# Performance work log

Measured on AMD Instinct MI355X. Metric: run time of the kernel, lower is better.

## Reference

```python
import jax, jax.numpy as jnp
import numpy as np

SIZE_DICT = 1024
DIM_DICT = 256
BETA = 0.001


def setup_inputs() -> dict:
    key = jax.random.key(0)
    k1, k2 = jax.random.split(key)
    z = jax.random.normal(k1, (64, 1024, DIM_DICT), dtype=jnp.float32)
    codebook = jax.random.normal(k2, (SIZE_DICT, DIM_DICT), dtype=jnp.float32)
    return {"z": z, "codebook": codebook, "flg_train": 1}


def reference(z, codebook, flg_train):
    zf = z.reshape(-1, DIM_DICT)  # [N, D]
    # squared euclidean distances: ||z||^2 + ||c||^2 - 2 z c^T  -> [N, K]
    d = (jnp.sum(zf ** 2, axis=1, keepdims=True)
         + jnp.sum(codebook ** 2, axis=1)
         - 2.0 * jnp.matmul(zf, codebook.T))
    idx = jnp.argmin(d, axis=1)  # [N]
    # one-hot @ codebook == gather
    z_q = codebook[idx].reshape(z.shape)
    if flg_train:
        loss = (jnp.mean((jax.lax.stop_gradient(z_q) - z) ** 2)
                + BETA * jnp.mean((z_q - jax.lax.stop_gradient(z)) ** 2))
    else:
        loss = jnp.float32(0.0)
    # straight-through estimator
    z_q = z + jax.lax.stop_gradient(z_q - z)
    # perplexity from codebook usage histogram (== mean of one-hot rows)
    n = zf.shape[0]
    counts = jax.ops.segment_sum(jnp.ones((n,), jnp.float32), idx,
                                 num_segments=SIZE_DICT)
    e_mean = counts / n
    perplexity = jnp.exp(-jnp.sum(e_mean * jnp.log(e_mean + 1e-10)))
    return (z_q, loss, perplexity)
```

## Files before the change

kernel.cpp:

```cpp
#include <hip/hip_runtime.h>


#define N_ROWS 65536
#define DIM    256
#define K_CODES 1024
#define BETA   0.001f

#define BM      128
#define NBLOCKS (N_ROWS / BM)
#define NTHREADS 512
#define STAGE_BYTES 32768
#define NSTAGE  32

#define LO_SCALE 2048.0f
#define LO_INV   (1.0f / 2048.0f)

#define WS_CBIMG_OFF 16384
#define WS_NEED (WS_CBIMG_OFF + NSTAGE * STAGE_BYTES)

typedef _Float16 f16x8 __attribute__((ext_vector_type(8)));
typedef float f32x16 __attribute__((ext_vector_type(16)));


__global__ void cnorm_kernel(const float* __restrict__ cb, float* __restrict__ cnorm) {
    int k = blockIdx.x * blockDim.x + threadIdx.x;
    if (k >= K_CODES) return;
    const float4* row = (const float4*)(cb + (size_t)k * DIM);
    float s = 0.f;
#pragma unroll
    for (int j = 0; j < DIM / 4; ++j) {
        float4 v = row[j];
        s = fmaf(v.x, v.x, s);
        s = fmaf(v.y, v.y, s);
        s = fmaf(v.z, v.z, s);
        s = fmaf(v.w, v.w, s);
    }
    cnorm[k] = s;
}

__global__ void cb_prep(const float* __restrict__ cb, char* __restrict__ img) {
    int idx = blockIdx.x * blockDim.x + threadIdx.x;
    int c   = idx >> 5;
    int g32 = idx & 31;
    const float4* src = (const float4*)(cb + (size_t)c * DIM + g32 * 8);
    float4 v0 = src[0], v1 = src[1];
    float vv[8] = {v0.x, v0.y, v0.z, v0.w, v1.x, v1.y, v1.z, v1.w};
    f16x8 hi, lo;
#pragma unroll
    for (int j = 0; j < 8; ++j) {
        _Float16 h = (_Float16)vv[j];
        hi[j] = h;
        lo[j] = (_Float16)((vv[j] - (float)h) * LO_SCALE);
    }
    int kh = g32 >> 4;
    int gl = g32 & 15;
    int cl = c & 63;
    int gp = gl ^ (cl & 7);
    int unit = (c >> 6) * 2 + kh;
    size_t off = (size_t)unit * STAGE_BYTES + (size_t)cl * 256 + (size_t)gp * 16;
    *(f16x8*)(img + off) = hi;
    *(f16x8*)(img + off + 16384) = lo;
}


__device__ inline void stage_unit(const char* img, int u, char* ldsbase, int tid) {
#pragma unroll
    for (int i = 0; i < 4; ++i) {
        __builtin_amdgcn_global_load_lds(
            (const __attribute__((address_space(1))) unsigned int*)
                (img + (size_t)u * STAGE_BYTES + i * 8192 + tid * 16),
            (__attribute__((address_space(3))) unsigned int*)
                (ldsbase + i * 8192 + tid * 16),
            16, 0, 0);
    }
}

#define COMPUTE_HALF(KH, BUF)                                                        \
    {                                                                                \
        const _Float16* ch_row = csb + (BUF) * 16384 + crow * 128;                   \
        const _Float16* cl_row = ch_row + 8192;                                      \
        _Pragma("unroll")                                                            \
        for (int ks = 0; ks < 8; ++ks) {                                             \
            int gb = (ks * 2 + lh) ^ csw;                                            \
            f16x8 bh = *(const f16x8*)(ch_row + gb * 8);                             \
            f16x8 bl = *(const f16x8*)(cl_row + gb * 8);                             \
            f16x8 ah = zh[(KH) * 8 + ks];                                            \
            f16x8 al = zl[(KH) * 8 + ks];                                            \
            acc_hh = __builtin_amdgcn_mfma_f32_32x32x16_f16(ah, bh, acc_hh, 0, 0, 0);\
            f32x16& ax = (ks & 1) ? acc_xo : acc_xe;                                 \
            ax = __builtin_amdgcn_mfma_f32_32x32x16_f16(ah, bl, ax, 0, 0, 0);        \
            ax = __builtin_amdgcn_mfma_f32_32x32x16_f16(al, bh, ax, 0, 0, 0);        \
        }                                                                            \
    }

__global__ __launch_bounds__(NTHREADS, 2)
void vq_main_mfma(const float* __restrict__ z, const float* __restrict__ cb,
                  const char* __restrict__ img, const float* __restrict__ cnorm,
                  float* __restrict__ out, int* __restrict__ counts,
                  float* __restrict__ ploss) {
    __shared__ _Float16 csb[2 * 16384];
    __shared__ unsigned long long bkey2[BM][2];
    __shared__ int bests[BM];
    __shared__ float red[NTHREADS];

    const int tid  = threadIdx.x;
    const int lane = tid & 63;
    const int w    = tid >> 6;
    const int wr   = w >> 1;
    const int wc   = w & 1;
    const int l31  = lane & 31;
    const int lh   = lane >> 5;
    const int r0   = blockIdx.x * BM;

    stage_unit(img, 0, (char*)csb, tid);

    const int zrow = wr * 32 + l31;
    f16x8 zh[16], zl[16];
    {
        const float* zr = z + (size_t)(r0 + zrow) * DIM;
#pragma unroll
        for (int gi = 0; gi < 16; ++gi) {
            int g = gi * 2 + lh;
            float4 v0 = *(const float4*)(zr + g * 8);
            float4 v1 = *(const float4*)(zr + g * 8 + 4);
            float vv[8] = {v0.x, v0.y, v0.z, v0.w, v1.x, v1.y, v1.z, v1.w};
            f16x8 hi, lo;
#pragma unroll
            for (int j = 0; j < 8; ++j) {
                _Float16 h = (_Float16)vv[j];
                hi[j] = h;
                lo[j] = (_Float16)((vv[j] - (float)h) * LO_SCALE);
            }
            zh[gi] = hi;
            zl[gi] = lo;
        }
    }

    f32x16 acc_hh, acc_xe, acc_xo;
#pragma unroll
    for (int e = 0; e < 16; ++e) { acc_hh[e] = 0.f; acc_xe[e] = 0.f; acc_xo[e] = 0.f; }
    unsigned long long bestk[16];
#pragma unroll
    for (int e = 0; e < 16; ++e) bestk[e] = ~0ull;

    const int crow = wc * 32 + l31;
    const int csw  = crow & 7;

#pragma unroll 1
    for (int chunk = 0; chunk < 16; ++chunk) {
        asm volatile("" ::: "memory");
        __builtin_amdgcn_s_barrier();
        asm volatile("" ::: "memory");
        stage_unit(img, 2 * chunk + 1, (char*)csb + 32768, tid);
        asm volatile("s_waitcnt vmcnt(4)" ::: "memory");
        __builtin_amdgcn_s_barrier();
        asm volatile("" ::: "memory");
        __builtin_amdgcn_s_setprio(1);
        COMPUTE_HALF(0, 0)
        __builtin_amdgcn_s_setprio(0);

        asm volatile("" ::: "memory");
        __builtin_amdgcn_s_barrier();
        asm volatile("" ::: "memory");
        if (chunk + 1 < 16) {
            stage_unit(img, 2 * chunk + 2, (char*)csb, tid);
            asm volatile("s_waitcnt vmcnt(4)" ::: "memory");
        } else {
            asm volatile("s_waitcnt vmcnt(0)" ::: "memory");
        }
        __builtin_amdgcn_s_barrier();
        asm volatile("" ::: "memory");
        __builtin_amdgcn_s_setprio(1);
        COMPUTE_HALF(1, 1)
        __builtin_amdgcn_s_setprio(0);

        {
            int col = chunk * 64 + wc * 32 + l31;
            float cn = cnorm[col];
#pragma unroll
            for (int rg = 0; rg < 16; ++rg) {
                float dot = fmaf(acc_xe[rg] + acc_xo[rg], LO_INV, acc_hh[rg]);
                float s = fmaf(-2.0f, dot, cn);
                unsigned uu = __float_as_uint(s);
                uu = (uu & 0x80000000u) ? ~uu : (uu | 0x80000000u);
                unsigned long long key = ((unsigned long long)uu << 32) | (unsigned)col;
                bestk[rg] = key < bestk[rg] ? key : bestk[rg];
            }
#pragma unroll
            for (int e = 0; e < 16; ++e) { acc_hh[e] = 0.f; acc_xe[e] = 0.f; acc_xo[e] = 0.f; }
        }
    }

#pragma unroll
    for (int rg = 0; rg < 16; ++rg) {
        unsigned long long bk = bestk[rg];
#pragma unroll
        for (int s = 1; s < 32; s <<= 1) {
            unsigned long long o = __shfl_xor(bk, s, 64);
            bk = o < bk ? o : bk;
        }
        bestk[rg] = bk;
    }
    if (l31 == 0) {
#pragma unroll
        for (int rg = 0; rg < 16; ++rg) {
            int rl = (rg & 3) + 8 * (rg >> 2) + 4 * lh;
            bkey2[wr * 32 + rl][wc] = bestk[rg];
        }
    }
    __syncthreads();
    if (tid < BM) {
        unsigned long long a = bkey2[tid][0];
        unsigned long long b2 = bkey2[tid][1];
        bests[tid] = (int)((a < b2 ? a : b2) & 0xffffffffu);
    }
    __syncthreads();

    const int r = tid >> 2;
    const int q = tid & 3;
    const int bidx = bests[r];
    const float* crow_g = cb + (size_t)bidx * DIM;
    const float* zrow_g = z + (size_t)(r0 + r) * DIM;
    float* orow = out + (size_t)(r0 + r) * DIM;
    float lsum = 0.f;
#pragma unroll
    for (int j = 0; j < 16; ++j) {
        int g4 = j * 4 + q;
        float4 c4 = *(const float4*)(crow_g + g4 * 4);
        float4 z4 = *(const float4*)(zrow_g + g4 * 4);
        float4 o;
        float dx = c4.x - z4.x; o.x = z4.x + dx; lsum = fmaf(dx, dx, lsum);
        float dy = c4.y - z4.y; o.y = z4.y + dy; lsum = fmaf(dy, dy, lsum);
        float dz = c4.z - z4.z; o.z = z4.z + dz; lsum = fmaf(dz, dz, lsum);
        float dw = c4.w - z4.w; o.w = z4.w + dw; lsum = fmaf(dw, dw, lsum);
        *(float4*)(orow + g4 * 4) = o;
    }
    if (tid < BM) atomicAdd(&counts[bests[tid]], 1);

    red[tid] = lsum;
    __syncthreads();
    for (int s = NTHREADS / 2; s > 0; s >>= 1) {
        if (tid < s) red[tid] += red[tid + s];
        __syncthreads();
    }
    if (tid == 0) ploss[blockIdx.x] = red[0];
}


#define FBM     32
#define FCHUNK  512
#define FDSTAGE 16
#define FCS_PAD 20
#define FNBLOCKS (N_ROWS / FBM)

__global__ __launch_bounds__(256, 2)
void vq_main_fp32(const float* __restrict__ z, const float* __restrict__ cb,
                  const float* __restrict__ cnorm, float* __restrict__ out,
                  int* __restrict__ counts, float* __restrict__ ploss) {
    __shared__ float zs[FBM][DIM];
    __shared__ float cs[FCHUNK][FCS_PAD];
    __shared__ int   bests[FBM];
    __shared__ float red[256];

    const int tid = threadIdx.x;
    const int tx  = tid & 63;
    const int ty  = tid >> 6;
    const int r0  = blockIdx.x * FBM;

    {
        const float4* zg  = (const float4*)(z + (size_t)r0 * DIM);
        float4*       zsv = (float4*)&zs[0][0];
#pragma unroll
        for (int j = 0; j < (FBM * DIM / 4) / 256; ++j)
            zsv[tid + 256 * j] = zg[tid + 256 * j];
    }

    unsigned long long best[8];
#pragma unroll
    for (int i = 0; i < 8; ++i) best[i] = ~0ull;

    for (int cb0 = 0; cb0 < K_CODES; cb0 += FCHUNK) {
        float acc[8][8];
#pragma unroll
        for (int i = 0; i < 8; ++i)
#pragma unroll
            for (int m = 0; m < 8; ++m) acc[i][m] = 0.f;

        for (int sd = 0; sd < DIM / FDSTAGE; ++sd) {
            __syncthreads();
#pragma unroll
            for (int j = 0; j < 8; ++j) {
                int f4i = tid + 256 * j;
                int c   = f4i >> 2;
                int qq  = f4i & 3;
                float4 v = *(const float4*)(cb + (size_t)(cb0 + c) * DIM + sd * FDSTAGE + qq * 4);
                *(float4*)&cs[c][qq * 4] = v;
            }
            __syncthreads();

#pragma unroll
            for (int dd4 = 0; dd4 < FDSTAGE / 4; ++dd4) {
                float4 zv[8], cv[8];
#pragma unroll
                for (int i = 0; i < 8; ++i)
                    zv[i] = *(const float4*)&zs[ty * 8 + i][sd * FDSTAGE + dd4 * 4];
#pragma unroll
                for (int m = 0; m < 8; ++m)
                    cv[m] = *(const float4*)&cs[tx + 64 * m][dd4 * 4];
#pragma unroll
                for (int i = 0; i < 8; ++i)
#pragma unroll
                    for (int m = 0; m < 8; ++m) {
                        float a = acc[i][m];
                        a = fmaf(zv[i].x, cv[m].x, a);
                        a = fmaf(zv[i].y, cv[m].y, a);
                        a = fmaf(zv[i].z, cv[m].z, a);
                        a = fmaf(zv[i].w, cv[m].w, a);
                        acc[i][m] = a;
                    }
            }
        }

#pragma unroll
        for (int m = 0; m < 8; ++m) {
            int   c  = cb0 + tx + 64 * m;
            float cn = cnorm[c];
#pragma unroll
            for (int i = 0; i < 8; ++i) {
                float s = fmaf(-2.f, acc[i][m], cn);
                unsigned u = __float_as_uint(s);
                u = (u & 0x80000000u) ? ~u : (u | 0x80000000u);
                unsigned long long key = ((unsigned long long)u << 32) | (unsigned)c;
                best[i] = key < best[i] ? key : best[i];
            }
        }
    }

#pragma unroll
    for (int i = 0; i < 8; ++i) {
        unsigned long long b = best[i];
#pragma unroll
        for (int s = 1; s < 64; s <<= 1) {
            unsigned long long o = __shfl_xor(b, s, 64);
            b = o < b ? o : b;
        }
        best[i] = b;
    }
    if (tx == 0)
#pragma unroll
        for (int i = 0; i < 8; ++i)
            bests[ty * 8 + i] = (int)(best[i] & 0xFFFFFFFFu);
    __syncthreads();

    const int r  = tid >> 3;
    const int lq = tid & 7;
    const int bidx = bests[r];
    const float4* crow = (const float4*)(cb + (size_t)bidx * DIM);
    const float4* zrow = (const float4*)&zs[r][0];
    float4*       orow = (float4*)(out + (size_t)(r0 + r) * DIM);
    float lsum = 0.f;
#pragma unroll
    for (int j = 0; j < 8; ++j) {
        int qg = lq + j * 8;
        float4 c4 = crow[qg];
        float4 z4 = zrow[qg];
        float4 o;
        float dx = c4.x - z4.x; o.x = z4.x + dx; lsum = fmaf(dx, dx, lsum);
        float dy = c4.y - z4.y; o.y = z4.y + dy; lsum = fmaf(dy, dy, lsum);
        float dz = c4.z - z4.z; o.z = z4.z + dz; lsum = fmaf(dz, dz, lsum);
        float dw = c4.w - z4.w; o.w = z4.w + dw; lsum = fmaf(dw, dw, lsum);
        orow[qg] = o;
    }
    if (tid < FBM) atomicAdd(&counts[bests[tid]], 1);

    red[tid] = lsum;
    __syncthreads();
    for (int s = 128; s > 0; s >>= 1) {
        if (tid < s) red[tid] += red[tid + s];
        __syncthreads();
    }
    if (tid == 0) ploss[blockIdx.x] = red[0];
}


__global__ void vq_final(const float* __restrict__ ploss, const int* __restrict__ counts,
                         const int* __restrict__ flg, float* __restrict__ out2, int np) {
    __shared__ float red[1024];
    const int t = threadIdx.x;

    float l = 0.f;
    for (int i = t; i < np; i += 1024) l += ploss[i];
    red[t] = l;
    __syncthreads();
    for (int s = 512; s > 0; s >>= 1) {
        if (t < s) red[t] += red[t + s];
        __syncthreads();
    }
    if (t == 0) {
        float loss = (red[0] / (float)((size_t)N_ROWS * DIM)) * (1.0f + BETA);
        if (flg[0] == 0) loss = 0.f;
        out2[0] = loss;
    }
    __syncthreads();

    float e = (float)counts[t] / (float)N_ROWS;
    red[t] = e * logf(e + 1e-10f);
    __syncthreads();
    for (int s = 512; s > 0; s >>= 1) {
        if (t < s) red[t] += red[t + s];
        __syncthreads();
    }
    if (t == 0) out2[1] = expf(-red[0]);
}

extern "C" void kernel_launch(void* const* d_in, const int* in_sizes, int n_in,
                              void* d_out, int out_size, void* d_ws, size_t ws_size,
                              hipStream_t stream) {
    const float* z   = (const float*)d_in[0];
    const float* cb  = (const float*)d_in[1];
    const int*   flg = (const int*)d_in[2];
    float* out = (float*)d_out;
    float* ws  = (float*)d_ws;

    float* cnorm  = ws;
    int*   counts = (int*)(ws + 1024);
    float* ploss  = ws + 2048;
    char*  cbimg  = (char*)d_ws + WS_CBIMG_OFF;

    hipMemsetAsync(counts, 0, K_CODES * sizeof(int), stream);
    cnorm_kernel<<<K_CODES / 256, 256, 0, stream>>>(cb, cnorm);

    if (ws_size >= (size_t)WS_NEED) {
        cb_prep<<<128, 256, 0, stream>>>(cb, cbimg);
        vq_main_mfma<<<NBLOCKS, NTHREADS, 0, stream>>>(z, cb, cbimg, cnorm, out, counts, ploss);
        vq_final<<<1, 1024, 0, stream>>>(ploss, counts, flg, out + (size_t)N_ROWS * DIM, NBLOCKS);
    } else {
        vq_main_fp32<<<FNBLOCKS, 256, 0, stream>>>(z, cb, cnorm, out, counts, ploss);
        vq_final<<<1, 1024, 0, stream>>>(ploss, counts, flg, out + (size_t)N_ROWS * DIM, FNBLOCKS);
    }
}
```

Measured before the change: 182.1 us.

## Load codebook MFMA operands directly from global memory instead of LDS staging

Removes the double-buffered LDS staging of the fp16 hi/lo codebook image, along with its barriers and global_load_lds calls. Each wave now reads its B operands straight from global memory (L2/L1 cached) in a coalesced column-major layout, loading all 8 k-slices ahead of the MFMA chain. This drops block-wide synchronisation and the LDS footprint, which could raise occupancy. The cost is exposed global and L2 latency on every chunk with no software prefetch, and redundant codebook fetches across waves.

Measured after the change: 225.7 us. 23.9% more time.

```diff
diff --git a/kernel.cpp b/kernel.cpp
--- a/kernel.cpp
+++ b/kernel.cpp
@@ -9,14 +9,13 @@
 #define BM      128
 #define NBLOCKS (N_ROWS / BM)
 #define NTHREADS 512
-#define STAGE_BYTES 32768
-#define NSTAGE  32
+#define UNIT_BYTES 32768
 
 #define LO_SCALE 2048.0f
 #define LO_INV   (1.0f / 2048.0f)
 
 #define WS_CBIMG_OFF 16384
-#define WS_NEED (WS_CBIMG_OFF + NSTAGE * STAGE_BYTES)
+#define WS_NEED (WS_CBIMG_OFF + 32 * UNIT_BYTES)
 
 typedef _Float16 f16x8 __attribute__((ext_vector_type(8)));
 typedef float f32x16 __attribute__((ext_vector_type(16)));
@@ -55,41 +54,31 @@
     int kh = g32 >> 4;
     int gl = g32 & 15;
     int cl = c & 63;
-    int gp = gl ^ (cl & 7);
     int unit = (c >> 6) * 2 + kh;
-    size_t off = (size_t)unit * STAGE_BYTES + (size_t)cl * 256 + (size_t)gp * 16;
+    size_t off = (size_t)unit * UNIT_BYTES + (size_t)gl * 2048 + (size_t)cl * 16;
     *(f16x8*)(img + off) = hi;
-    *(f16x8*)(img + off + 16384) = lo;
-}
-
-
-__device__ inline void stage_unit(const char* img, int u, char* ldsbase, int tid) {
-#pragma unroll
-    for (int i = 0; i < 4; ++i) {
-        __builtin_amdgcn_global_load_lds(
-            (const __attribute__((address_space(1))) unsigned int*)
-                (img + (size_t)u * STAGE_BYTES + i * 8192 + tid * 16),
-            (__attribute__((address_space(3))) unsigned int*)
-                (ldsbase + i * 8192 + tid * 16),
-            16, 0, 0);
-    }
-}
-
-#define COMPUTE_HALF(KH, BUF)                                                        \
+    *(f16x8*)(img + off + 1024) = lo;
+}
+
+
+#define COMPUTE_HALF(KH)                                                             \
     {                                                                                \
-        const _Float16* ch_row = csb + (BUF) * 16384 + crow * 128;                   \
-        const _Float16* cl_row = ch_row + 8192;                                      \
+        const char* ub = img + (size_t)(chunk * 2 + (KH)) * UNIT_BYTES + crow16;     \
+        f16x8 bh[8], bl[8];                                                          \
         _Pragma("unroll")                                                            \
         for (int ks = 0; ks < 8; ++ks) {                                             \
-            int gb = (ks * 2 + lh) ^ csw;                                            \
-            f16x8 bh = *(const f16x8*)(ch_row + gb * 8);                             \
-            f16x8 bl = *(const f16x8*)(cl_row + gb * 8);                             \
+            int g = ks * 2 + lh;                                                     \
+            bh[ks] = *(const f16x8*)(ub + g * 2048);                                 \
+            bl[ks] = *(const f16x8*)(ub + g * 2048 + 1024);                          \
+        }                                                                            \
+        _Pragma("unroll")                                                            \
+        for (int ks = 0; ks < 8; ++ks) {                                             \
             f16x8 ah = zh[(KH) * 8 + ks];                                            \
             f16x8 al = zl[(KH) * 8 + ks];                                            \
-            acc_hh = __builtin_amdgcn_mfma_f32_32x32x16_f16(ah, bh, acc_hh, 0, 0, 0);\
+            acc_hh = __builtin_amdgcn_mfma_f32_32x32x16_f16(ah, bh[ks], acc_hh, 0, 0, 0); \
             f32x16& ax = (ks & 1) ? acc_xo : acc_xe;                                 \
-            ax = __builtin_amdgcn_mfma_f32_32x32x16_f16(ah, bl, ax, 0, 0, 0);        \
-            ax = __builtin_amdgcn_mfma_f32_32x32x16_f16(al, bh, ax, 0, 0, 0);        \
+            ax = __builtin_amdgcn_mfma_f32_32x32x16_f16(ah, bl[ks], ax, 0, 0, 0);    \
+            ax = __builtin_amdgcn_mfma_f32_32x32x16_f16(al, bh[ks], ax, 0, 0, 0);    \
         }                                                                            \
     }
 
@@ -98,7 +87,6 @@
                   const char* __restrict__ img, const float* __restrict__ cnorm,
                   float* __restrict__ out, int* __restrict__ counts,
                   float* __restrict__ ploss) {
-    __shared__ _Float16 csb[2 * 16384];
     __shared__ unsigned long long bkey2[BM][2];
     __shared__ int bests[BM];
     __shared__ float red[NTHREADS];
@@ -112,8 +100,6 @@
     const int lh   = lane >> 5;
     const int r0   = blockIdx.x * BM;
 
-    stage_unit(img, 0, (char*)csb, tid);
-
     const int zrow = wr * 32 + l31;
     f16x8 zh[16], zl[16];
     {
@@ -144,51 +130,27 @@
     for (int e = 0; e < 16; ++e) bestk[e] = ~0ull;
 
     const int crow = wc * 32 + l31;
-    const int csw  = crow & 7;
+    const int crow16 = crow * 16;
 
 #pragma unroll 1
     for (int chunk = 0; chunk < 16; ++chunk) {
-        asm volatile("" ::: "memory");
-        __builtin_amdgcn_s_barrier();
-        asm volatile("" ::: "memory");
-        stage_unit(img, 2 * chunk + 1, (char*)csb + 32768, tid);
-        asm volatile("s_waitcnt vmcnt(4)" ::: "memory");
-        __builtin_amdgcn_s_barrier();
-        asm volatile("" ::: "memory");
-        __builtin_amdgcn_s_setprio(1);
-        COMPUTE_HALF(0, 0)
-        __builtin_amdgcn_s_setprio(0);
-
-        asm volatile("" ::: "memory");
-        __builtin_amdgcn_s_barrier();
-        asm volatile("" ::: "memory");
-        if (chunk + 1 < 16) {
-            stage_unit(img, 2 * chunk + 2, (char*)csb, tid);
-            asm volatile("s_waitcnt vmcnt(4)" ::: "memory");
-        } else {
-            asm volatile("s_waitcnt vmcnt(0)" ::: "memory");
-        }
-        __builtin_amdgcn_s_barrier();
-        asm volatile("" ::: "memory");
-        __builtin_amdgcn_s_setprio(1);
-        COMPUTE_HALF(1, 1)
-        __builtin_amdgcn_s_setprio(0);
-
-        {
-            int col = chunk * 64 + wc * 32 + l31;
-            float cn = cnorm[col];
-#pragma unroll
-            for (int rg = 0; rg < 16; ++rg) {
-                float dot = fmaf(acc_xe[rg] + acc_xo[rg], LO_INV, acc_hh[rg]);
-                float s = fmaf(-2.0f, dot, cn);
-                unsigned uu = __float_as_uint(s);
-                uu = (uu & 0x80000000u) ? ~uu : (uu | 0x80000000u);
-                unsigned long long key = ((unsigned long long)uu << 32) | (unsigned)col;
-                bestk[rg] = key < bestk[rg] ? key : bestk[rg];
-            }
-#pragma unroll
-            for (int e = 0; e < 16; ++e) { acc_hh[e] = 0.f; acc_xe[e] = 0.f; acc_xo[e] = 0.f; }
-        }
+        int col = chunk * 64 + crow;
+        float cn = cnorm[col];
+
+        COMPUTE_HALF(0)
+        COMPUTE_HALF(1)
+
+#pragma unroll
+        for (int rg = 0; rg < 16; ++rg) {
+            float dot = fmaf(acc_xe[rg] + acc_xo[rg], LO_INV, acc_hh[rg]);
+            float s = fmaf(-2.0f, dot, cn);
+            unsigned uu = __float_as_uint(s);
+            uu = (uu & 0x80000000u) ? ~uu : (uu | 0x80000000u);
+            unsigned long long key = ((unsigned long long)uu << 32) | (unsigned)col;
+            bestk[rg] = key < bestk[rg] ? key : bestk[rg];
+        }
+#pragma unroll
+        for (int e = 0; e < 16; ++e) { acc_hh[e] = 0.f; acc_xe[e] = 0.f; acc_xo[e] = 0.f; }
     }
 
 #pragma unroll
```

## Halve row tile, stage codebook in quarter units, raise occupancy

Applied to the files above, without the earlier changes.

Shrinks the row block from 128 to 64 rows with 256 threads and targets 3 blocks per CU. The codebook image is relaid into 16KB quarter-K units, so the double buffer uses half the LDS and the main loop runs 64 fine-grained stages. The two cross-term accumulators are merged into one, and the packed 64-bit argmin key is replaced by a separate float score and int index. The aim is better latency hiding from higher occupancy, at the cost of twice as many codebook passes across blocks and longer MFMA dependency chains. Because the loop is not unrolled, the z fragments are indexed by the runtime value u&3, which may push them out of registers into scratch.

After: 442.9 us. 143% more time.

```diff
diff --git a/kernel.cpp b/kernel.cpp
--- a/kernel.cpp
+++ b/kernel.cpp
@@ -6,17 +6,17 @@
 #define K_CODES 1024
 #define BETA   0.001f
 
-#define BM      128
+#define BM      64
 #define NBLOCKS (N_ROWS / BM)
-#define NTHREADS 512
-#define STAGE_BYTES 32768
-#define NSTAGE  32
+#define NTHREADS 256
+#define QUNIT_BYTES 16384
+#define NQUNIT  64
 
 #define LO_SCALE 2048.0f
 #define LO_INV   (1.0f / 2048.0f)
 
 #define WS_CBIMG_OFF 16384
-#define WS_NEED (WS_CBIMG_OFF + NSTAGE * STAGE_BYTES)
+#define WS_NEED (WS_CBIMG_OFF + NQUNIT * QUNIT_BYTES)
 
 typedef _Float16 f16x8 __attribute__((ext_vector_type(8)));
 typedef float f32x16 __attribute__((ext_vector_type(16)));
@@ -52,55 +52,38 @@
         hi[j] = h;
         lo[j] = (_Float16)((vv[j] - (float)h) * LO_SCALE);
     }
-    int kh = g32 >> 4;
-    int gl = g32 & 15;
-    int cl = c & 63;
-    int gp = gl ^ (cl & 7);
-    int unit = (c >> 6) * 2 + kh;
-    size_t off = (size_t)unit * STAGE_BYTES + (size_t)cl * 256 + (size_t)gp * 16;
+    int q    = g32 >> 3;
+    int grel = g32 & 7;
+    int cl   = c & 63;
+    int gp   = grel ^ (cl & 7);
+    int qunit = (c >> 6) * 4 + q;
+    size_t off = (size_t)qunit * QUNIT_BYTES + (size_t)cl * 128 + (size_t)gp * 16;
     *(f16x8*)(img + off) = hi;
-    *(f16x8*)(img + off + 16384) = lo;
-}
-
-
-__device__ inline void stage_unit(const char* img, int u, char* ldsbase, int tid) {
+    *(f16x8*)(img + off + 8192) = lo;
+}
+
+
+__device__ inline void stage_q(const char* img, int u, char* ldsbase, int tid) {
 #pragma unroll
     for (int i = 0; i < 4; ++i) {
         __builtin_amdgcn_global_load_lds(
             (const __attribute__((address_space(1))) unsigned int*)
-                (img + (size_t)u * STAGE_BYTES + i * 8192 + tid * 16),
+                (img + (size_t)u * QUNIT_BYTES + i * 4096 + tid * 16),
             (__attribute__((address_space(3))) unsigned int*)
-                (ldsbase + i * 8192 + tid * 16),
+                (ldsbase + i * 4096 + tid * 16),
             16, 0, 0);
     }
 }
 
-#define COMPUTE_HALF(KH, BUF)                                                        \
-    {                                                                                \
-        const _Float16* ch_row = csb + (BUF) * 16384 + crow * 128;                   \
-        const _Float16* cl_row = ch_row + 8192;                                      \
-        _Pragma("unroll")                                                            \
-        for (int ks = 0; ks < 8; ++ks) {                                             \
-            int gb = (ks * 2 + lh) ^ csw;                                            \
-            f16x8 bh = *(const f16x8*)(ch_row + gb * 8);                             \
-            f16x8 bl = *(const f16x8*)(cl_row + gb * 8);                             \
-            f16x8 ah = zh[(KH) * 8 + ks];                                            \
-            f16x8 al = zl[(KH) * 8 + ks];                                            \
-            acc_hh = __builtin_amdgcn_mfma_f32_32x32x16_f16(ah, bh, acc_hh, 0, 0, 0);\
-            f32x16& ax = (ks & 1) ? acc_xo : acc_xe;                                 \
-            ax = __builtin_amdgcn_mfma_f32_32x32x16_f16(ah, bl, ax, 0, 0, 0);        \
-            ax = __builtin_amdgcn_mfma_f32_32x32x16_f16(al, bh, ax, 0, 0, 0);        \
-        }                                                                            \
-    }
-
-__global__ __launch_bounds__(NTHREADS, 2)
+__global__ __launch_bounds__(NTHREADS, 3)
 void vq_main_mfma(const float* __restrict__ z, const float* __restrict__ cb,
                   const char* __restrict__ img, const float* __restrict__ cnorm,
                   float* __restrict__ out, int* __restrict__ counts,
                   float* __restrict__ ploss) {
-    __shared__ _Float16 csb[2 * 16384];
-    __shared__ unsigned long long bkey2[BM][2];
-    __shared__ int bests[BM];
+    __shared__ _Float16 csb[2 * 8192];
+    __shared__ float bs2[BM][2];
+    __shared__ int   bc2[BM][2];
+    __shared__ int   bests[BM];
     __shared__ float red[NTHREADS];
 
     const int tid  = threadIdx.x;
@@ -112,7 +95,7 @@
     const int lh   = lane >> 5;
     const int r0   = blockIdx.x * BM;
 
-    stage_unit(img, 0, (char*)csb, tid);
+    stage_q(img, 0, (char*)csb, tid);
 
     const int zrow = wr * 32 + l31;
     f16x8 zh[16], zl[16];
@@ -136,88 +119,99 @@
         }
     }
 
-    f32x16 acc_hh, acc_xe, acc_xo;
-#pragma unroll
-    for (int e = 0; e < 16; ++e) { acc_hh[e] = 0.f; acc_xe[e] = 0.f; acc_xo[e] = 0.f; }
-    unsigned long long bestk[16];
-#pragma unroll
-    for (int e = 0; e < 16; ++e) bestk[e] = ~0ull;
+    f32x16 acc_hh, acc_x;
+#pragma unroll
+    for (int e = 0; e < 16; ++e) { acc_hh[e] = 0.f; acc_x[e] = 0.f; }
+    float best_s[16];
+    int   best_c[16];
+#pragma unroll
+    for (int e = 0; e < 16; ++e) { best_s[e] = 3.4e38f; best_c[e] = 0; }
 
     const int crow = wc * 32 + l31;
     const int csw  = crow & 7;
 
 #pragma unroll 1
-    for (int chunk = 0; chunk < 16; ++chunk) {
+    for (int u = 0; u < NQUNIT; ++u) {
+        const int b = u & 1;
         asm volatile("" ::: "memory");
         __builtin_amdgcn_s_barrier();
         asm volatile("" ::: "memory");
-        stage_unit(img, 2 * chunk + 1, (char*)csb + 32768, tid);
-        asm volatile("s_waitcnt vmcnt(4)" ::: "memory");
-        __builtin_amdgcn_s_barrier();
-        asm volatile("" ::: "memory");
-        __builtin_amdgcn_s_setprio(1);
-        COMPUTE_HALF(0, 0)
-        __builtin_amdgcn_s_setprio(0);
-
-        asm volatile("" ::: "memory");
-        __builtin_amdgcn_s_barrier();
-        asm volatile("" ::: "memory");
-        if (chunk + 1 < 16) {
-            stage_unit(img, 2 * chunk + 2, (char*)csb, tid);
+        if (u + 1 < NQUNIT) {
+            stage_q(img, u + 1, (char*)csb + (b ^ 1) * QUNIT_BYTES, tid);
             asm volatile("s_waitcnt vmcnt(4)" ::: "memory");
         } else {
             asm volatile("s_waitcnt vmcnt(0)" ::: "memory");
         }
         __builtin_amdgcn_s_barrier();
         asm volatile("" ::: "memory");
+
+        const int q = u & 3;
+        const _Float16* ch_row = csb + b * 8192 + crow * 64;
+        const _Float16* cl_row = ch_row + 4096;
+
         __builtin_amdgcn_s_setprio(1);
-        COMPUTE_HALF(1, 1)
+#pragma unroll
+        for (int ks = 0; ks < 4; ++ks) {
+            int gb = (ks * 2 + lh) ^ csw;
+            f16x8 bh = *(const f16x8*)(ch_row + gb * 8);
+            f16x8 bl = *(const f16x8*)(cl_row + gb * 8);
+            f16x8 ah = zh[q * 4 + ks];
+            f16x8 al = zl[q * 4 + ks];
+            acc_hh = __builtin_amdgcn_mfma_f32_32x32x16_f16(ah, bh, acc_hh, 0, 0, 0);
+            acc_x  = __builtin_amdgcn_mfma_f32_32x32x16_f16(ah, bl, acc_x, 0, 0, 0);
+            acc_x  = __builtin_amdgcn_mfma_f32_32x32x16_f16(al, bh, acc_x, 0, 0, 0);
+        }
         __builtin_amdgcn_s_setprio(0);
 
-        {
-            int col = chunk * 64 + wc * 32 + l31;
+        if (q == 3) {
+            int col = (u >> 2) * 64 + crow;
             float cn = cnorm[col];
 #pragma unroll
             for (int rg = 0; rg < 16; ++rg) {
-                float dot = fmaf(acc_xe[rg] + acc_xo[rg], LO_INV, acc_hh[rg]);
-                float s = fmaf(-2.0f, dot, cn);
-                unsigned uu = __float_as_uint(s);
-                uu = (uu & 0x80000000u) ? ~uu : (uu | 0x80000000u);
-                unsigned long long key = ((unsigned long long)uu << 32) | (unsigned)col;
-                bestk[rg] = key < bestk[rg] ? key : bestk[rg];
+                float s = fmaf(-2.0f, fmaf(acc_x[rg], LO_INV, acc_hh[rg]), cn);
+                bool take = s < best_s[rg];
+                best_s[rg] = take ? s : best_s[rg];
+                best_c[rg] = take ? col : best_c[rg];
             }
 #pragma unroll
-            for (int e = 0; e < 16; ++e) { acc_hh[e] = 0.f; acc_xe[e] = 0.f; acc_xo[e] = 0.f; }
+            for (int e = 0; e < 16; ++e) { acc_hh[e] = 0.f; acc_x[e] = 0.f; }
         }
     }
 
 #pragma unroll
     for (int rg = 0; rg < 16; ++rg) {
-        unsigned long long bk = bestk[rg];
+        float bsv = best_s[rg];
+        int   bcv = best_c[rg];
 #pragma unroll
         for (int s = 1; s < 32; s <<= 1) {
-            unsigned long long o = __shfl_xor(bk, s, 64);
-            bk = o < bk ? o : bk;
-        }
-        bestk[rg] = bk;
+            float os = __shfl_xor(bsv, s, 64);
+            int   oc = __shfl_xor(bcv, s, 64);
+            bool take = (os < bsv) || (os == bsv && oc < bcv);
+            bsv = take ? os : bsv;
+            bcv = take ? oc : bcv;
+        }
+        best_s[rg] = bsv;
+        best_c[rg] = bcv;
     }
     if (l31 == 0) {
 #pragma unroll
         for (int rg = 0; rg < 16; ++rg) {
             int rl = (rg & 3) + 8 * (rg >> 2) + 4 * lh;
-            bkey2[wr * 32 + rl][wc] = bestk[rg];
+            bs2[wr * 32 + rl][wc] = best_s[rg];
+            bc2[wr * 32 + rl][wc] = best_c[rg];
         }
     }
     __syncthreads();
     if (tid < BM) {
-        unsigned long long a = bkey2[tid][0];
-        unsigned long long b2 = bkey2[tid][1];
-        bests[tid] = (int)((a < b2 ? a : b2) & 0xffffffffu);
+        float s0 = bs2[tid][0], s1 = bs2[tid][1];
+        int   c0 = bc2[tid][0], c1 = bc2[tid][1];
+        bool take1 = (s1 < s0) || (s1 == s0 && c1 < c0);
+        bests[tid] = take1 ? c1 : c0;
     }
     __syncthreads();
 
     const int r = tid >> 2;
-    const int q = tid & 3;
+    const int q4 = tid & 3;
     const int bidx = bests[r];
     const float* crow_g = cb + (size_t)bidx * DIM;
     const float* zrow_g = z + (size_t)(r0 + r) * DIM;
@@ -225,7 +219,7 @@
     float lsum = 0.f;
 #pragma unroll
     for (int j = 0; j < 16; ++j) {
-        int g4 = j * 4 + q;
+        int g4 = j * 4 + q4;
         float4 c4 = *(const float4*)(crow_g + g4 * 4);
         float4 z4 = *(const float4*)(zrow_g + g4 * 4);
         float4 o;
```
